# Performance work log

Hardware: AMD Instinct MI355X
Metric: run time of the kernel (lower is better)

## Reference

```python
import jax, jax.numpy as jnp
import numpy as np

N_HEADS = 16
N_KV_HEADS = 4
HEAD_DIM = 128
ROPE_THETA = 10000.0


def _rope_cos_sin(seq_len, head_dim, dtype):
    inv_freq = 1.0 / (ROPE_THETA ** (jnp.arange(0, head_dim, 2, dtype=jnp.float32) / head_dim))
    angles = jnp.arange(seq_len, dtype=jnp.float32)[:, None] * inv_freq[None, :]  # [S, hd/2]
    return jnp.cos(angles).astype(dtype), jnp.sin(angles).astype(dtype)


def _apply_rope(t, cos, sin):
    # t: [B, S, H, hd]; interleaved-pair (complex) rotation, Llama style
    B, S, H, hd = t.shape
    tr = t.reshape(B, S, H, hd // 2, 2)
    t0, t1 = tr[..., 0], tr[..., 1]
    c = cos[None, :, None, :]
    s = sin[None, :, None, :]
    out = jnp.stack([t0 * c - t1 * s, t0 * s + t1 * c], axis=-1)
    return out.reshape(B, S, H, hd)


def setup_inputs() -> dict:
    key = jax.random.key(0)
    ks = jax.random.split(key, 5)
    B, S, D = 2, 2048, 2048
    scale = 0.02
    return {
        "x": jax.random.normal(ks[0], (B, S, D), dtype=jnp.float32),
        "wq": jax.random.normal(ks[1], (N_HEADS * HEAD_DIM, D), dtype=jnp.float32) * scale,
        "wk": jax.random.normal(ks[2], (N_KV_HEADS * HEAD_DIM, D), dtype=jnp.float32) * scale,
        "wv": jax.random.normal(ks[3], (N_KV_HEADS * HEAD_DIM, D), dtype=jnp.float32) * scale,
        "wo": jax.random.normal(ks[4], (D, N_HEADS * HEAD_DIM), dtype=jnp.float32) * scale,
    }


def reference(x, wq, wk, wv, wo):
    B, S, D = x.shape
    hd = HEAD_DIM
    # QKV projections (torch Linear: y = x @ W.T)
    q = (x @ wq.T).reshape(B, S, N_HEADS, hd)
    k = (x @ wk.T).reshape(B, S, N_KV_HEADS, hd)
    v = (x @ wv.T).reshape(B, S, N_KV_HEADS, hd)
    # RoPE on q, k
    cos, sin = _rope_cos_sin(S, hd, x.dtype)
    q = _apply_rope(q, cos, sin)
    k = _apply_rope(k, cos, sin)
    # GQA: repeat kv heads to match query heads
    rep = N_HEADS // N_KV_HEADS
    k = jnp.repeat(k, rep, axis=2)  # [B, S, H, hd]
    v = jnp.repeat(v, rep, axis=2)
    # Causal SDPA
    scores = jnp.einsum("bqhd,bkhd->bhqk", q, k) / jnp.sqrt(jnp.asarray(hd, x.dtype))
    causal = jnp.tril(jnp.ones((S, S), dtype=bool))
    scores = jnp.where(causal[None, None], scores, jnp.asarray(-1e30, x.dtype))
    attn = jax.nn.softmax(scores, axis=-1)
    out = jnp.einsum("bhqk,bkhd->bqhd", attn, v).reshape(B, S, N_HEADS * hd)
    return out @ wo.T
```

## Files before the change

kernel.cpp:

```cpp
#include <hip/hip_runtime.h>
#include <stdint.h>

typedef unsigned short u16;
typedef __attribute__((ext_vector_type(8))) __bf16 bf16x8;
typedef __attribute__((ext_vector_type(4))) float f32x4;

__device__ __forceinline__ u16 f2bf(float f) {
  union { float f; uint32_t u; } v; v.f = f;
  uint32_t u = v.u;
  uint32_t r = (u + 0x7fffu + ((u >> 16) & 1u)) >> 16;
  return (u16)r;
}
__device__ __forceinline__ float bf2f(u16 h) {
  union { uint32_t u; float f; } v; v.u = ((uint32_t)h) << 16;
  return v.f;
}

__device__ __forceinline__ void gld16(const void* g, void* l) {
  __builtin_amdgcn_global_load_lds(
      (__attribute__((address_space(1))) void*)(uintptr_t)g,
      (__attribute__((address_space(3))) void*)l,
      16, 0, 0);
}

__device__ __forceinline__ void xcd_supertile(int& bm, int& bn) {
  int flat = blockIdx.y * gridDim.x + blockIdx.x;
  if (gridDim.y == 32 && (gridDim.x & 3) == 0) {
    int xcd = flat & 7;
    int c   = flat >> 3;
    int st  = c >> 4;
    int r   = c & 15;
    bm = xcd * 4 + (r >> 2);
    bn = st * 4 + (r & 3);
  } else {
    bm = flat / gridDim.x;
    bn = flat % gridDim.x;
  }
}

__global__ __launch_bounds__(256) void cast_all(const float* __restrict__ x,
                                                const float* __restrict__ wq,
                                                const float* __restrict__ wk,
                                                const float* __restrict__ wv,
                                                const float* __restrict__ wo,
                                                u16* __restrict__ xb,
                                                u16* __restrict__ wqkv,
                                                u16* __restrict__ wob) {
  for (int i = blockIdx.x * 256 + threadIdx.x; i < 4718592; i += 2048 * 256) {
    const float* src; u16* dst; int loc, base;
    if (i < 2097152)      { src = x;  dst = xb;   loc = i;           base = 0; }
    else if (i < 3145728) { src = wq; dst = wqkv; loc = i - 2097152; base = 0; }
    else if (i < 3407872) { src = wk; dst = wqkv; loc = i - 3145728; base = 1048576; }
    else if (i < 3670016) { src = wv; dst = wqkv; loc = i - 3407872; base = 1310720; }
    else                  { src = wo; dst = wob;  loc = i - 3670016; base = 0; }
    float4 f = ((const float4*)src)[loc];
    ushort4 o;
    o.x = f2bf(f.x); o.y = f2bf(f.y); o.z = f2bf(f.z); o.w = f2bf(f.w);
    ((ushort4*)dst)[base + loc] = o;
  }
}

__global__ __launch_bounds__(256) void gemm_bt(const u16* __restrict__ A,
                                               const u16* __restrict__ B,
                                               void* __restrict__ C,
                                               u16* __restrict__ Vtg,
                                               int M, int N, int K, int out_f32,
                                               int do_rope)
{
  __shared__ u16 As[128 * 64];
  __shared__ u16 Bs[128 * 64];
  const int tid  = threadIdx.x;
  const int wave = tid >> 6, lane = tid & 63;
  const int col  = lane & 15, quad = lane >> 4;

  int bm, bn;
  xcd_supertile(bm, bn);

  const int wm = (wave >> 1) * 64, wn = (wave & 1) * 64;
  const size_t arow0 = (size_t)bm * 128, brow0 = (size_t)bn * 128;

  const int sr = lane >> 3, pc = lane & 7;

  const f32x4 fz = {0.f, 0.f, 0.f, 0.f};
  f32x4 acc[4][4];
  for (int i = 0; i < 4; ++i)
    for (int j = 0; j < 4; ++j) acc[i][j] = fz;

  for (int k0 = 0; k0 < K; k0 += 64) {
    __syncthreads();
    #pragma unroll
    for (int i = 0; i < 4; ++i) {
      int rA = wave * 32 + i * 8 + sr;
      int lc = pc ^ (rA & 7);
      gld16(A + (arow0 + rA) * K + k0 + lc * 8, As + (wave * 32 + i * 8) * 64);
      gld16(B + (brow0 + rA) * K + k0 + lc * 8, Bs + (wave * 32 + i * 8) * 64);
    }
    __syncthreads();
    #pragma unroll
    for (int kk = 0; kk < 2; ++kk) {
      const int swzk = (((kk * 4 + quad) ^ (col & 7)) * 8);
      bf16x8 af[4];
      #pragma unroll
      for (int mt = 0; mt < 4; ++mt)
        af[mt] = *(const bf16x8*)&As[(wm + mt * 16 + col) * 64 + swzk];
      #pragma unroll
      for (int nt = 0; nt < 4; ++nt) {
        bf16x8 bf = *(const bf16x8*)&Bs[(wn + nt * 16 + col) * 64 + swzk];
        #pragma unroll
        for (int mt = 0; mt < 4; ++mt)
          acc[mt][nt] = __builtin_amdgcn_mfma_f32_16x16x32_bf16(af[mt], bf, acc[mt][nt], 0, 0, 0);
      }
    }
  }

  const float qscale = 0.12751744515623627f;
  #pragma unroll
  for (int mt = 0; mt < 4; ++mt)
    #pragma unroll
    for (int nt = 0; nt < 4; ++nt) {
      const size_t gcol = brow0 + wn + nt * 16 + col;
      const bool v_here    = do_rope && (gcol >= 2560);
      const bool rope_here = do_rope && (gcol < 2560);
      const int  d    = (int)(gcol & 127);
      const float osc = (gcol < 2048) ? qscale : 1.0f;
      const float inv = exp2f(-(float)(d >> 1) * 0.20762050593046f);
      const bool odd  = (d & 1) != 0;
      if (v_here) {
        const int vc  = (int)gcol - 2560;
        const int kvh = vc >> 7;
        const size_t grow0 = arow0 + wm + mt * 16 + quad * 4;
        const int bb = (int)(grow0 >> 11);
        const int s0 = (int)(grow0 & 2047);
        ushort4 o4;
        o4.x = f2bf(acc[mt][nt][0]);
        o4.y = f2bf(acc[mt][nt][1]);
        o4.z = f2bf(acc[mt][nt][2]);
        o4.w = f2bf(acc[mt][nt][3]);
        *(ushort4*)&Vtg[((size_t)((bb * 4 + kvh) * 128 + d)) * 2048 + s0] = o4;
        continue;
      }
      #pragma unroll
      for (int i = 0; i < 4; ++i) {
        size_t grow = arow0 + wm + mt * 16 + quad * 4 + i;
        float v = acc[mt][nt][i];
        if (rope_here) {
          float p = __shfl_xor(v, 1);
          float ang = (float)(int)(grow & 2047) * inv;
          float sn, cs;
          __sincosf(ang, &sn, &cs);
          v = odd ? (p * sn + v * cs) * osc : (v * cs - p * sn) * osc;
        }
        if (out_f32) ((float*)C)[grow * N + gcol] = v;
        else         ((u16*)C)[grow * N + gcol]   = f2bf(v);
      }
    }
}

__global__ __launch_bounds__(256) void gemm_bt_dbuf(const u16* __restrict__ A,
                                                    const u16* __restrict__ B,
                                                    float* __restrict__ C,
                                                    int M, int N, int K)
{
  __shared__ u16 As[2][128 * 64];
  __shared__ u16 Bs[2][128 * 64];
  const int tid  = threadIdx.x;
  const int wave = tid >> 6, lane = tid & 63;
  const int col  = lane & 15, quad = lane >> 4;

  int bm, bn;
  xcd_supertile(bm, bn);

  const int wm = (wave >> 1) * 64, wn = (wave & 1) * 64;
  const size_t arow0 = (size_t)bm * 128, brow0 = (size_t)bn * 128;
  const int sr = lane >> 3, pc = lane & 7;

  const f32x4 fz = {0.f, 0.f, 0.f, 0.f};
  f32x4 acc[4][4];
  for (int i = 0; i < 4; ++i)
    for (int j = 0; j < 4; ++j) acc[i][j] = fz;

  #pragma unroll
  for (int i = 0; i < 4; ++i) {
    int rA = wave * 32 + i * 8 + sr;
    int lc = pc ^ (rA & 7);
    gld16(A + (arow0 + rA) * K + lc * 8, As[0] + (wave * 32 + i * 8) * 64);
    gld16(B + (brow0 + rA) * K + lc * 8, Bs[0] + (wave * 32 + i * 8) * 64);
  }

  const int T = K / 64;
  for (int t = 0; t < T; ++t) {
    __syncthreads();
    if (t + 1 < T) {
      const int k0 = (t + 1) * 64;
      u16* ad = As[(t + 1) & 1];
      u16* bd = Bs[(t + 1) & 1];
      #pragma unroll
      for (int i = 0; i < 4; ++i) {
        int rA = wave * 32 + i * 8 + sr;
        int lc = pc ^ (rA & 7);
        gld16(A + (arow0 + rA) * K + k0 + lc * 8, ad + (wave * 32 + i * 8) * 64);
        gld16(B + (brow0 + rA) * K + k0 + lc * 8, bd + (wave * 32 + i * 8) * 64);
      }
    }
    const u16* Ac = As[t & 1];
    const u16* Bc = Bs[t & 1];
    #pragma unroll
    for (int kk = 0; kk < 2; ++kk) {
      const int swzk = (((kk * 4 + quad) ^ (col & 7)) * 8);
      bf16x8 af[4];
      #pragma unroll
      for (int mt = 0; mt < 4; ++mt)
        af[mt] = *(const bf16x8*)&Ac[(wm + mt * 16 + col) * 64 + swzk];
      #pragma unroll
      for (int nt = 0; nt < 4; ++nt) {
        bf16x8 bf = *(const bf16x8*)&Bc[(wn + nt * 16 + col) * 64 + swzk];
        #pragma unroll
        for (int mt = 0; mt < 4; ++mt)
          acc[mt][nt] = __builtin_amdgcn_mfma_f32_16x16x32_bf16(af[mt], bf, acc[mt][nt], 0, 0, 0);
      }
    }
  }

  #pragma unroll
  for (int mt = 0; mt < 4; ++mt)
    #pragma unroll
    for (int nt = 0; nt < 4; ++nt)
      #pragma unroll
      for (int i = 0; i < 4; ++i) {
        size_t grow = arow0 + wm + mt * 16 + quad * 4 + i;
        size_t gcol = brow0 + wn + nt * 16 + col;
        C[grow * N + gcol] = acc[mt][nt][i];
      }
}

__global__ __launch_bounds__(512, 4) void attn_kernel(const u16* __restrict__ QKV,
                                                      const u16* __restrict__ Vtg,
                                                      u16* __restrict__ Ctx,
                                                      int B, int S)
{
  const int x = blockIdx.x;
  const int t = x >> 5, bh = x & 31;
  const int qt = (x < 256) ? (15 - t) : (t - 8);
  const int h = bh & 15, b = bh >> 4;
  const int tid  = threadIdx.x;
  const int wave = tid >> 6, lane = tid & 63;
  const int col  = lane & 15, quad = lane >> 4;
  const int q0   = qt * 128;
  const int kvh  = h >> 2;
  const int row0w = q0 + wave * 16;

  __shared__ u16 Ks[64 * 128];
  __shared__ u16 Vt[128 * 64];
  __shared__ u16 Ps[8][16 * 72];

  bf16x8 aq[4];
  #pragma unroll
  for (int ks = 0; ks < 4; ++ks)
    aq[ks] = *(const bf16x8*)(QKV + (size_t)(b * S + row0w + col) * 3072
                                  + h * 128 + ks * 32 + quad * 8);

  const u16* KVb = QKV + (size_t)b * S * 3072 + 2048 + kvh * 128;
  const u16* Vtb = Vtg + ((size_t)(b * 4 + kvh) * 128) * S;
  u16* Pw = Ps[wave];

  const f32x4 fz = {0.f, 0.f, 0.f, 0.f};
  f32x4 o[8];
  #pragma unroll
  for (int nc = 0; nc < 8; ++nc) o[nc] = fz;
  float rs = 0.f;

  const int kt_max = 2 * qt + 1;

  for (int kt = 0; kt <= kt_max; ++kt) {
    __syncthreads();
    #pragma unroll
    for (int i = 0; i < 2; ++i) {
      int r = wave * 8 + i * 4 + (lane >> 4);
      int lc = (lane & 15) ^ (r & 15);
      gld16(KVb + (size_t)(kt * 64 + r) * 3072 + lc * 8, Ks + (wave * 8 + i * 4) * 128);
    }
    #pragma unroll
    for (int i = 0; i < 2; ++i) {
      int r = wave * 16 + i * 8 + (lane >> 3);
      int lc = (lane & 7) ^ (r & 7);
      gld16(Vtb + (size_t)r * S + kt * 64 + lc * 8, Vt + (wave * 16 + i * 8) * 64);
    }
    __syncthreads();

    if (kt * 64 > row0w + 15) continue;
    const bool need_mask = (kt * 64 + 63 > row0w);

    #pragma unroll
    for (int nt = 0; nt < 4; ++nt) {
      bf16x8 kA[4];
      #pragma unroll
      for (int ks = 0; ks < 4; ++ks)
        kA[ks] = *(const bf16x8*)&Ks[(nt * 16 + col) * 128 + (((ks * 4 + quad) ^ col) * 8)];
      f32x4 st = fz;
      #pragma unroll
      for (int ks = 0; ks < 4; ++ks)
        st = __builtin_amdgcn_mfma_f32_16x16x32_bf16(kA[ks], aq[ks], st, 0, 0, 0);
      float pv[4];
      const int kbase = kt * 64 + nt * 16 + quad * 4;
      const int qrow  = row0w + col;
      #pragma unroll
      for (int i = 0; i < 4; ++i) {
        float s = st[i];
        if (need_mask && (kbase + i > qrow)) s = -__builtin_inff();
        pv[i] = exp2f(s);
      }
      rs += (pv[0] + pv[1]) + (pv[2] + pv[3]);
      uint32_t d0 = (__float_as_uint(pv[0]) >> 16) | (__float_as_uint(pv[1]) & 0xffff0000u);
      uint32_t d1 = (__float_as_uint(pv[2]) >> 16) | (__float_as_uint(pv[3]) & 0xffff0000u);
      uint2 dd; dd.x = d0; dd.y = d1;
      *(uint2*)&Pw[col * 72 + nt * 16 + quad * 4] = dd;
    }
    __asm__ volatile("" ::: "memory");

    bf16x8 ap[2];
    #pragma unroll
    for (int ks = 0; ks < 2; ++ks)
      ap[ks] = *(const bf16x8*)&Pw[col * 72 + ks * 32 + quad * 8];
    #pragma unroll
    for (int nc = 0; nc < 8; ++nc) {
      #pragma unroll
      for (int ks = 0; ks < 2; ++ks) {
        bf16x8 bv = *(const bf16x8*)&Vt[(nc * 16 + col) * 64 + (((ks * 4 + quad) ^ (col & 7)) * 8)];
        o[nc] = __builtin_amdgcn_mfma_f32_16x16x32_bf16(ap[ks], bv, o[nc], 0, 0, 0);
      }
    }
  }

  {
    float v = rs;
    v += __shfl_xor(v, 16);
    v += __shfl_xor(v, 32);
    float lv[4];
    #pragma unroll
    for (int i = 0; i < 4; ++i)
      lv[i] = 1.0f / __shfl(v, quad * 4 + i);
    #pragma unroll
    for (int nc = 0; nc < 8; ++nc)
      #pragma unroll
      for (int i = 0; i < 4; ++i) {
        int qg = row0w + quad * 4 + i;
        Ctx[(size_t)(b * S + qg) * 2048 + h * 128 + nc * 16 + col] =
            f2bf(o[nc][i] * lv[i]);
      }
  }
}

extern "C" void kernel_launch(void* const* d_in, const int* in_sizes, int n_in,
                              void* d_out, int out_size, void* d_ws, size_t ws_size,
                              hipStream_t stream) {
  const int B = 2, S = 2048, D = 2048;
  const int M = B * S;
  const int NQKV = 3072;

  const float* x  = (const float*)d_in[0];
  const float* wq = (const float*)d_in[1];
  const float* wk = (const float*)d_in[2];
  const float* wv = (const float*)d_in[3];
  const float* wo = (const float*)d_in[4];

  char* ws = (char*)d_ws;
  u16* xb    = (u16*)ws; ws += (size_t)M * D * 2;
  u16* wqkvb = (u16*)ws; ws += (size_t)NQKV * D * 2;
  u16* wob   = (u16*)ws; ws += (size_t)D * D * 2;
  u16* qkvb  = (u16*)ws; ws += (size_t)M * NQKV * 2;
  u16* vtg   = (u16*)ws; ws += (size_t)B * 4 * 128 * S * 2;
  u16* ctx   = (u16*)ws; ws += (size_t)M * D * 2;

  cast_all<<<2048, 256, 0, stream>>>(x, wq, wk, wv, wo, xb, wqkvb, wob);

  gemm_bt<<<dim3(NQKV / 128, M / 128), 256, 0, stream>>>(xb, wqkvb, qkvb, vtg, M, NQKV, D, 0, 1);

  attn_kernel<<<512, 512, 0, stream>>>(qkvb, vtg, ctx, B, S);

  gemm_bt_dbuf<<<dim3(D / 128, M / 128), 256, 0, stream>>>(ctx, wob, (float*)d_out, M, D, D);
}
```

Baseline: 281.1 us.

## Double-buffer K/V tiles in LDS and swizzle the P scratch buffer

Keeps two LDS copies of the K and V^T tiles and prefetches tile kt+1 while tile kt is computed. This removes one of the two barriers per iteration and hides global-load latency behind the MFMA work. The padded P staging buffer (stride 72) becomes an XOR-swizzled stride-64 layout to avoid bank conflicts with less memory, and an empty asm pins the Q fragments in registers. The larger LDS footprint, roughly 80KB per block, lowers how many blocks fit on a CU.

```diff
diff --git a/kernel.cpp b/kernel.cpp
--- a/kernel.cpp
+++ b/kernel.cpp
@@ -249,15 +249,18 @@
   const int kvh  = h >> 2;
   const int row0w = q0 + wave * 16;
 
-  __shared__ u16 Ks[64 * 128];
-  __shared__ u16 Vt[128 * 64];
-  __shared__ u16 Ps[8][16 * 72];
+  __shared__ u16 Ks[2][64 * 128];
+  __shared__ u16 Vt[2][128 * 64];
+  __shared__ u16 Ps[8][16 * 64];
 
   bf16x8 aq[4];
   #pragma unroll
   for (int ks = 0; ks < 4; ++ks)
     aq[ks] = *(const bf16x8*)(QKV + (size_t)(b * S + row0w + col) * 3072
                                   + h * 128 + ks * 32 + quad * 8);
+  #pragma unroll
+  for (int ks = 0; ks < 4; ++ks)
+    asm volatile("" :: "v"(__builtin_bit_cast(f32x4, aq[ks])));
 
   const u16* KVb = QKV + (size_t)b * S * 3072 + 2048 + kvh * 128;
   const u16* Vtb = Vtg + ((size_t)(b * 4 + kvh) * 128) * S;
@@ -271,31 +274,52 @@
 
   const int kt_max = 2 * qt + 1;
 
+  #pragma unroll
+  for (int i = 0; i < 2; ++i) {
+    int r = wave * 8 + i * 4 + (lane >> 4);
+    int lc = (lane & 15) ^ (r & 15);
+    gld16(KVb + (size_t)r * 3072 + lc * 8, Ks[0] + (wave * 8 + i * 4) * 128);
+  }
+  #pragma unroll
+  for (int i = 0; i < 2; ++i) {
+    int r = wave * 16 + i * 8 + (lane >> 3);
+    int lc = (lane & 7) ^ (r & 7);
+    gld16(Vtb + (size_t)r * S + lc * 8, Vt[0] + (wave * 16 + i * 8) * 64);
+  }
+
   for (int kt = 0; kt <= kt_max; ++kt) {
     __syncthreads();
-    #pragma unroll
-    for (int i = 0; i < 2; ++i) {
-      int r = wave * 8 + i * 4 + (lane >> 4);
-      int lc = (lane & 15) ^ (r & 15);
-      gld16(KVb + (size_t)(kt * 64 + r) * 3072 + lc * 8, Ks + (wave * 8 + i * 4) * 128);
-    }
-    #pragma unroll
-    for (int i = 0; i < 2; ++i) {
-      int r = wave * 16 + i * 8 + (lane >> 3);
-      int lc = (lane & 7) ^ (r & 7);
-      gld16(Vtb + (size_t)r * S + kt * 64 + lc * 8, Vt + (wave * 16 + i * 8) * 64);
-    }
-    __syncthreads();
+
+    if (kt < kt_max) {
+      u16* kd = Ks[(kt + 1) & 1];
+      u16* vd = Vt[(kt + 1) & 1];
+      #pragma unroll
+      for (int i = 0; i < 2; ++i) {
+        int r = wave * 8 + i * 4 + (lane >> 4);
+        int lc = (lane & 15) ^ (r & 15);
+        gld16(KVb + (size_t)((kt + 1) * 64 + r) * 3072 + lc * 8,
+              kd + (wave * 8 + i * 4) * 128);
+      }
+      #pragma unroll
+      for (int i = 0; i < 2; ++i) {
+        int r = wave * 16 + i * 8 + (lane >> 3);
+        int lc = (lane & 7) ^ (r & 7);
+        gld16(Vtb + (size_t)r * S + (kt + 1) * 64 + lc * 8,
+              vd + (wave * 16 + i * 8) * 64);
+      }
+    }
 
     if (kt * 64 > row0w + 15) continue;
     const bool need_mask = (kt * 64 + 63 > row0w);
+    const u16* Kc = Ks[kt & 1];
+    const u16* Vc = Vt[kt & 1];
 
     #pragma unroll
     for (int nt = 0; nt < 4; ++nt) {
       bf16x8 kA[4];
       #pragma unroll
       for (int ks = 0; ks < 4; ++ks)
-        kA[ks] = *(const bf16x8*)&Ks[(nt * 16 + col) * 128 + (((ks * 4 + quad) ^ col) * 8)];
+        kA[ks] = *(const bf16x8*)&Kc[(nt * 16 + col) * 128 + (((ks * 4 + quad) ^ col) * 8)];
       f32x4 st = fz;
       #pragma unroll
       for (int ks = 0; ks < 4; ++ks)
@@ -313,19 +337,20 @@
       uint32_t d0 = (__float_as_uint(pv[0]) >> 16) | (__float_as_uint(pv[1]) & 0xffff0000u);
       uint32_t d1 = (__float_as_uint(pv[2]) >> 16) | (__float_as_uint(pv[3]) & 0xffff0000u);
       uint2 dd; dd.x = d0; dd.y = d1;
-      *(uint2*)&Pw[col * 72 + nt * 16 + quad * 4] = dd;
+      const int g8 = nt * 4 + quad;
+      *(uint2*)&Pw[col * 64 + ((g8 ^ ((col & 7) << 1)) << 2)] = dd;
     }
     __asm__ volatile("" ::: "memory");
 
     bf16x8 ap[2];
     #pragma unroll
     for (int ks = 0; ks < 2; ++ks)
-      ap[ks] = *(const bf16x8*)&Pw[col * 72 + ks * 32 + quad * 8];
+      ap[ks] = *(const bf16x8*)&Pw[col * 64 + (((ks * 4 + quad) ^ (col & 7)) << 3)];
     #pragma unroll
     for (int nc = 0; nc < 8; ++nc) {
       #pragma unroll
       for (int ks = 0; ks < 2; ++ks) {
-        bf16x8 bv = *(const bf16x8*)&Vt[(nc * 16 + col) * 64 + (((ks * 4 + quad) ^ (col & 7)) * 8)];
+        bf16x8 bv = *(const bf16x8*)&Vc[(nc * 16 + col) * 64 + (((ks * 4 + quad) ^ (col & 7)) * 8)];
         o[nc] = __builtin_amdgcn_mfma_f32_16x16x32_bf16(ap[ks], bv, o[nc], 0, 0, 0);
       }
     }
```

Measured after the change: 284.6 us. About the same (+1.2%).
